# Optimization experiments

Measured on AMD Instinct MI355X. Metric: run time of the kernel, lower is better.

Reference implementation:

```python
import jax, jax.numpy as jnp
import numpy as np


def setup_inputs() -> dict:
    key = jax.random.key(0)
    ks = jax.random.split(key, 9)
    B, C, H, W = 4, 256, 64, 64
    Ci = C // 2
    s = 0.05  # keep activations numerically tame
    return {
        "x": jax.random.normal(ks[0], (B, C, H, W), jnp.float32),
        "w_g": jax.random.normal(ks[1], (Ci, C), jnp.float32) * s,
        "b_g": jax.random.normal(ks[2], (Ci,), jnp.float32) * s,
        "w_theta": jax.random.normal(ks[3], (Ci, C), jnp.float32) * s,
        "b_theta": jax.random.normal(ks[4], (Ci,), jnp.float32) * s,
        "w_phi": jax.random.normal(ks[5], (Ci, C), jnp.float32) * s,
        "b_phi": jax.random.normal(ks[6], (Ci,), jnp.float32) * s,
        "w_out": jax.random.normal(ks[7], (C, Ci), jnp.float32) * s,
        "b_out": jax.random.normal(ks[8], (C,), jnp.float32) * s,
    }


def reference(x, w_g, b_g, w_theta, b_theta, w_phi, b_phi, w_out, b_out):
    B, C, H, W = x.shape
    Ci = w_g.shape[0]
    N = H * W
    xr = x.reshape(B, C, N)  # flatten spatial dims

    def proj(w, b):  # 1x1 conv == per-pixel GEMM
        return jnp.einsum("oc,bcn->bon", w, xr) + b[None, :, None]

    g_x = proj(w_g, b_g)          # [B, Ci, N]
    theta_x = proj(w_theta, b_theta)
    phi_x = proj(w_phi, b_phi)

    scale = jnp.asarray(Ci, x.dtype) ** 0.5
    f = jnp.einsum("bci,bcj->bij", theta_x, phi_x) / scale  # [B, N, N]
    attn = jax.nn.softmax(f, axis=-1)

    # out[b,c,i] = sum_j g_x[b,c,j] * attn[b,i,j]
    out = jnp.einsum("bcj,bij->bci", g_x, attn)             # [B, Ci, N]
    y = jnp.einsum("oc,bcn->bon", w_out, out) + b_out[None, :, None]
    return y.reshape(B, C, H, W) + x
```

## Files before the change

kernel.cpp:

```cpp
#include <hip/hip_runtime.h>
#include <hip/hip_bf16.h>


typedef float f32x4 __attribute__((ext_vector_type(4)));
typedef float f32x16 __attribute__((ext_vector_type(16)));
typedef short s16x8 __attribute__((ext_vector_type(8)));
typedef short s16x4 __attribute__((ext_vector_type(4)));

#define B_  4
#define C_  256
#define CI_ 128
#define N_  4096

#define OFF_Q    (8ull  << 20)
#define OFF_K    (12ull << 20)
#define OFF_G    (16ull << 20)
#define OFF_O    (20ull << 20)
#define OFF_WQK  (24ull << 20)
#define OFF_WG   (OFF_WQK + 131072)
#define OFF_WOUT (OFF_WG  + 65536)
#define OFF_BQK  (OFF_WOUT + 65536)
#define OFF_BG   (OFF_BQK + 1024)
#define OFF_BOUT (OFF_BG  + 512)
#define OFF_END  (OFF_BOUT + 1024)

__device__ inline f32x4 mfma16(s16x8 a, s16x8 b, f32x4 c) {
    return __builtin_amdgcn_mfma_f32_16x16x32_bf16(a, b, c, 0, 0, 0);
}
__device__ inline f32x16 mfma32(s16x8 a, s16x8 b, f32x16 c) {
    return __builtin_amdgcn_mfma_f32_32x32x16_bf16(a, b, c, 0, 0, 0);
}
__device__ inline f32x16 mfma32f8(long a, long b, f32x16 c) {
    return __builtin_amdgcn_mfma_f32_32x32x16_fp8_fp8(a, b, c, 0, 0, 0);
}
__device__ inline s16x8 ld8(const __hip_bfloat16* p) { return *(const s16x8*)p; }
__device__ inline float b2f(short u) {
    return __uint_as_float(((unsigned int)(unsigned short)u) << 16);
}
__device__ inline unsigned int pk2(float a, float b) {
    __hip_bfloat162 h;
    h.x = __float2bfloat16(a); h.y = __float2bfloat16(b);
    return *(unsigned int*)&h;
}
__device__ inline unsigned char f2fp8(float v) {
    int r = __builtin_amdgcn_cvt_pk_fp8_f32(v, v, 0, false);
    return (unsigned char)(r & 0xff);
}
__device__ inline void gload_lds16(const void* g, void* l) {
    __builtin_amdgcn_global_load_lds(
        (const __attribute__((address_space(1))) unsigned int*)g,
        (__attribute__((address_space(3))) unsigned int*)l, 16, 0, 0);
}
__device__ inline float fexp2(float x) { return __builtin_amdgcn_exp2f(x); }

__global__ void prep_weights(const float* wg, const float* bg,
                             const float* wt, const float* bt,
                             const float* wp, const float* bp,
                             const float* wo, const float* bo, char* ws) {
    __hip_bfloat16* Wqk  = (__hip_bfloat16*)(ws + OFF_WQK);
    __hip_bfloat16* Wg   = (__hip_bfloat16*)(ws + OFF_WG);
    __hip_bfloat16* Wout = (__hip_bfloat16*)(ws + OFF_WOUT);
    float* Bqk  = (float*)(ws + OFF_BQK);
    float* Bg   = (float*)(ws + OFF_BG);
    float* Bout = (float*)(ws + OFF_BOUT);
    const float rs16 = 0.08838834764831845f * 1.4426950408889634f * 16.0f;
    int idx = blockIdx.x * 256 + threadIdx.x;
    if (idx < 65536) {
        int r = idx >> 8, c = idx & 255;
        float v = (r < 128) ? wt[r * 256 + c] * rs16 : wp[(r - 128) * 256 + c];
        Wqk[idx] = __float2bfloat16(v);
    }
    if (idx < 32768) {
        Wg[idx]   = __float2bfloat16(wg[idx]);
        Wout[idx] = __float2bfloat16(wo[idx]);
    }
    if (idx < 256) { Bqk[idx] = (idx < 128) ? bt[idx] * rs16 : bp[idx - 128]; Bout[idx] = bo[idx]; }
    if (idx < 128) Bg[idx] = bg[idx];
}

__global__ __launch_bounds__(256) void proj(const float* x, char* ws) {
    const __hip_bfloat16* Wqk = (const __hip_bfloat16*)(ws + OFF_WQK);
    const __hip_bfloat16* Wg  = (const __hip_bfloat16*)(ws + OFF_WG);
    const float* Bqk = (const float*)(ws + OFF_BQK);
    const float* Bg  = (const float*)(ws + OFF_BG);
    unsigned char* Qf = (unsigned char*)(ws + OFF_Q);
    unsigned char* Kt = (unsigned char*)(ws + OFF_K);
    __hip_bfloat16* G = (__hip_bfloat16*)(ws + OFF_G);

    __shared__ char at[32 * 512];

    int b = blockIdx.y, n0 = blockIdx.x * 32;
    int t = threadIdx.x;
    int w = t >> 6, l = t & 63, lr = l & 15, lg = l >> 4;

    {
        int n4 = (t & 7) * 4;
        int cp = t >> 3;
        const float* xb = x + ((size_t)b * C_) * N_ + n0 + n4;
#pragma unroll
        for (int p = 0; p < 4; p++) {
            int c0 = (p * 32 + cp) * 2;
            f32x4 vA = *(const f32x4*)(xb + (size_t)c0 * N_);
            f32x4 vB = *(const f32x4*)(xb + (size_t)(c0 + 1) * N_);
            int slot = c0 >> 3, coff = (c0 & 7) << 1;
#pragma unroll
            for (int i = 0; i < 4; i++) {
                int n = n4 + i;
                *(unsigned int*)(&at[n * 512 + ((slot ^ (n & 7)) << 4) + coff]) =
                    pk2(vA[i], vB[i]);
            }
        }
    }
    __syncthreads();

    f32x4 acc[4][2] = {};
    f32x4 accg[2][2] = {};
    int o0q = w * 64, o0g = w * 32;
#pragma unroll
    for (int kk = 0; kk < 8; kk++) {
        s16x8 a[2];
#pragma unroll
        for (int nf = 0; nf < 2; nf++) {
            int row = nf * 16 + lr;
            int s = (4 * kk + lg) ^ (row & 7);
            a[nf] = *(const s16x8*)(&at[row * 512 + s * 16]);
        }
#pragma unroll
        for (int of = 0; of < 4; of++) {
            s16x8 bb = ld8(Wqk + (size_t)(o0q + 16 * of + lr) * C_ + kk * 32 + lg * 8);
            acc[of][0] = mfma16(a[0], bb, acc[of][0]);
            acc[of][1] = mfma16(a[1], bb, acc[of][1]);
        }
#pragma unroll
        for (int og = 0; og < 2; og++) {
            s16x8 ag = ld8(Wg + (size_t)(o0g + 16 * og + lr) * C_ + kk * 32 + lg * 8);
            accg[og][0] = mfma16(ag, a[0], accg[og][0]);
            accg[og][1] = mfma16(ag, a[1], accg[og][1]);
        }
    }
#pragma unroll
    for (int of = 0; of < 4; of++) {
        int o = o0q + 16 * of + lr;
        float bias = Bqk[o];
#pragma unroll
        for (int nf = 0; nf < 2; nf++) {
#pragma unroll
            for (int i = 0; i < 4; i++) {
                int n = n0 + 16 * nf + lg * 4 + i;
                float v = acc[of][nf][i] + bias;
                unsigned char u8 = f2fp8(v);
                if (o < 128) {
                    Qf[((size_t)b * N_ + n) * 128 + o] = u8;
                } else {
                    int op = o - 128;
                    size_t a2 = (((size_t)b * (N_ / 32) + (n >> 5)) << 12) +
                                ((op >> 3) << 8) + ((n & 31) << 3) + (op & 7);
                    Kt[a2] = u8;
                }
            }
        }
    }
#pragma unroll
    for (int og = 0; og < 2; og++) {
#pragma unroll
        for (int i = 0; i < 4; i++) {
            int o = o0g + 16 * og + lg * 4 + i;
            float bias = Bg[o];
#pragma unroll
            for (int nf = 0; nf < 2; nf++) {
                int n = n0 + 16 * nf + lr;
                G[(size_t)(b * CI_ + o) * N_ + n] = __float2bfloat16(accg[og][nf][i] + bias);
            }
        }
    }
}

__global__ __launch_bounds__(256, 4) void flashf8(char* ws, int nchunk,
                                                  unsigned long long off_part,
                                                  unsigned long long off_ml) {
    const unsigned char* Qf = (const unsigned char*)(ws + OFF_Q);
    const unsigned char* Kt = (const unsigned char*)(ws + OFF_K);
    const __hip_bfloat16* G = (const __hip_bfloat16*)(ws + OFF_G);
    __hip_bfloat16* OP = (__hip_bfloat16*)(ws + off_part);
    float* ML = (float*)(ws + off_ml);

    __shared__ char kbuf[2][4096];
    __shared__ char vbuf[2][128 * 64];

    int L = blockIdx.x;
    int npairs = B_ * nchunk;
    int pair = L % npairs, qt = L / npairs;
    int b = pair / nchunk, cz = pair % nchunk;
    int per = 128 / nchunk, rem = 128 % nchunk;
    int jb_t = per * cz + (cz < rem ? cz : rem);
    int sz_t = per + (cz < rem ? 1 : 0);
    int jb = jb_t << 5, je = jb + (sz_t << 5);

    int w = threadIdx.x >> 6, l = threadIdx.x & 63;
    int cl = l & 31, hi = l >> 5;
    int q0 = qt * 128 + w * 32;
    int vkey = (l >> 1) & 3;

    auto STAGE = [&](int pb_, int j0_) {
        {
            const char* src = (const char*)Kt +
                (((size_t)b * (N_ / 32) + (j0_ >> 5)) << 12) + w * 1024 + (l << 4);
            gload_lds16(src, &kbuf[pb_][w * 1024]);
        }
#pragma unroll
        for (int i = 0; i < 2; i++) {
            int c = w * 32 + i * 16 + (l >> 2);
            int srcslot = (l & 3) ^ ((l >> 3) & 3);
            const char* src = (const char*)G + ((((size_t)b * CI_ + c) * N_ + j0_) << 1)
                              + (srcslot << 4);
            gload_lds16(src, &vbuf[pb_][(w * 32 + i * 16) * 64]);
        }
    };

    long qf[8];
    {
        const char* qrow = (const char*)Qf + ((size_t)b * N_ + q0 + cl) * 128 + hi * 8;
#pragma unroll
        for (int st = 0; st < 8; st++) qf[st] = *(const long*)(qrow + st * 16);
    }

    f32x16 oacc[4] = {};
    float m_i = 0.f, lsum = 0.f, negmc = 0.f;

    STAGE(0, jb);
    __syncthreads();
    int pb = 0;

    for (int j0 = jb; j0 < je; j0 += 32) {
        if (j0 + 32 < je) STAGE(pb ^ 1, j0 + 32);
        const char* kb = kbuf[pb];
        const char* vbb = vbuf[pb];
        f32x16 s = {};
        __builtin_amdgcn_s_setprio(1);
#pragma unroll
        for (int st = 0; st < 8; st++) {
            long kf = *(const long*)(kb + (((st << 1) + hi) << 8) + (cl << 3));
            s = mfma32f8(kf, qf[st], s);
        }
        __builtin_amdgcn_s_setprio(0);
        if (j0 == jb) {
            float t0 = fmaxf(fmaxf(s[0], s[1]), fmaxf(s[2], s[3]));
            float t1 = fmaxf(fmaxf(s[4], s[5]), fmaxf(s[6], s[7]));
            float t2 = fmaxf(fmaxf(s[8], s[9]), fmaxf(s[10], s[11]));
            float t3 = fmaxf(fmaxf(s[12], s[13]), fmaxf(s[14], s[15]));
            float tm = fmaxf(fmaxf(t0, t1), fmaxf(t2, t3));
            tm = fmaxf(tm, __shfl_xor(tm, 32));
            m_i = tm;
            negmc = -m_i * 0.0625f;
        }
#pragma unroll
        for (int r = 0; r < 16; r++) s[r] = fexp2(fmaf(s[r], 0.0625f, negmc));
        lsum += ((s[0] + s[1]) + (s[2] + s[3])) + ((s[4] + s[5]) + (s[6] + s[7]))
              + ((s[8] + s[9]) + (s[10] + s[11])) + ((s[12] + s[13]) + (s[14] + s[15]));
        union { unsigned int u[4]; s16x8 v; } pa0, pa1;
#pragma unroll
        for (int i = 0; i < 4; i++) {
            pa0.u[i] = pk2(s[2 * i], s[2 * i + 1]);
            pa1.u[i] = pk2(s[8 + 2 * i], s[9 + 2 * i]);
        }
        __builtin_amdgcn_s_setprio(1);
#pragma unroll
        for (int u = 0; u < 2; u++) {
            s16x8 pa = u ? pa1.v : pa0.v;
#pragma unroll
            for (int cb = 0; cb < 4; cb++) {
                const char* base = vbb + ((cb * 32 + cl) << 6) + hi * 8;
                union { s16x4 h[2]; s16x8 v; } vf;
                vf.h[0] = *(const s16x4*)(base + ((((u << 1))     ^ vkey) << 4));
                vf.h[1] = *(const s16x4*)(base + ((((u << 1) | 1) ^ vkey) << 4));
                oacc[cb] = mfma32(pa, vf.v, oacc[cb]);
            }
        }
        __builtin_amdgcn_s_setprio(0);
        __syncthreads();
        pb ^= 1;
    }
    lsum += __shfl_xor(lsum, 32);
#pragma unroll
    for (int cb = 0; cb < 4; cb++) {
#pragma unroll
        for (int r = 0; r < 16; r++) {
            int q = q0 + (r & 3) + 8 * (r >> 2) + 4 * hi;
            OP[((size_t)(cz * B_ + b) * N_ + q) * CI_ + cb * 32 + cl] =
                __float2bfloat16(oacc[cb][r]);
        }
    }
    if (l < 32) {
        size_t mi = ((size_t)(cz * B_ + b) * N_ + q0 + l) * 2;
        ML[mi] = m_i * 0.0625f;
        ML[mi + 1] = lsum;
    }
}

template <int NC>
__global__ __launch_bounds__(256) void combine(char* ws,
                                               unsigned long long off_part,
                                               unsigned long long off_ml) {
    const __hip_bfloat16* OP = (const __hip_bfloat16*)(ws + off_part);
    const float* ML = (const float*)(ws + off_ml);
    __hip_bfloat16* O = (__hip_bfloat16*)(ws + OFF_O);
    int idx = blockIdx.x * 256 + threadIdx.x;
    int cg = idx & 15, n = (idx >> 4) & (N_ - 1), b = idx >> 16;
    float mz[NC], lz[NC], M = -1e30f;
#pragma unroll
    for (int z = 0; z < NC; z++) {
        size_t mi = ((size_t)(z * B_ + b) * N_ + n) * 2;
        mz[z] = ML[mi]; lz[z] = ML[mi + 1];
        M = fmaxf(M, mz[z]);
    }
    float Lsum = 0.f, wz[NC];
#pragma unroll
    for (int z = 0; z < NC; z++) { wz[z] = fexp2(mz[z] - M); Lsum += lz[z] * wz[z]; }
    float inv = 1.f / Lsum;
    float o[8] = {};
#pragma unroll
    for (int z = 0; z < NC; z++) {
        s16x8 v = ld8(OP + ((size_t)(z * B_ + b) * N_ + n) * CI_ + cg * 8);
        float wv = wz[z] * inv;
#pragma unroll
        for (int i = 0; i < 8; i++) o[i] += wv * b2f(v[i]);
    }
    s16x8 r;
#pragma unroll
    for (int i = 0; i < 8; i++) {
        __hip_bfloat16 h = __float2bfloat16(o[i]);
        r[i] = *(short*)&h;
    }
    *(s16x8*)(O + ((size_t)b * N_ + n) * CI_ + cg * 8) = r;
}

__global__ __launch_bounds__(256) void gemm_out(const float* x, char* ws, float* y) {
    const __hip_bfloat16* Ob = (const __hip_bfloat16*)(ws + OFF_O);
    const __hip_bfloat16* Wo = (const __hip_bfloat16*)(ws + OFF_WOUT);
    const float* Bout = (const float*)(ws + OFF_BOUT);
    int b = blockIdx.y;
    int w = threadIdx.x >> 6, l = threadIdx.x & 63, lr = l & 15, lg = l >> 4;
    int n0 = blockIdx.x * 32;
    int o0 = w * 64;
    f32x4 acc[4][2] = {};
#pragma unroll
    for (int kk = 0; kk < 4; kk++) {
        s16x8 bb[2];
#pragma unroll
        for (int nf = 0; nf < 2; nf++)
            bb[nf] = ld8(Ob + (size_t)(b * N_ + n0 + 16 * nf + lr) * CI_ + kk * 32 + lg * 8);
#pragma unroll
        for (int of = 0; of < 4; of++) {
            s16x8 a = ld8(Wo + (size_t)(o0 + 16 * of + lr) * CI_ + kk * 32 + lg * 8);
#pragma unroll
            for (int nf = 0; nf < 2; nf++)
                acc[of][nf] = mfma16(a, bb[nf], acc[of][nf]);
        }
    }
#pragma unroll
    for (int of = 0; of < 4; of++) {
#pragma unroll
        for (int i = 0; i < 4; i++) {
            int o = o0 + 16 * of + lg * 4 + i;
            float bias = Bout[o];
#pragma unroll
            for (int nf = 0; nf < 2; nf++) {
                int n = n0 + 16 * nf + lr;
                size_t idx = (size_t)(b * C_ + o) * N_ + n;
                y[idx] = acc[of][nf][i] + bias + x[idx];
            }
        }
    }
}

extern "C" void kernel_launch(void* const* d_in, const int* in_sizes, int n_in,
                              void* d_out, int out_size, void* d_ws, size_t ws_size,
                              hipStream_t stream) {
    const float* x  = (const float*)d_in[0];
    const float* wg = (const float*)d_in[1];
    const float* bg = (const float*)d_in[2];
    const float* wt = (const float*)d_in[3];
    const float* bt = (const float*)d_in[4];
    const float* wp = (const float*)d_in[5];
    const float* bp = (const float*)d_in[6];
    const float* wo = (const float*)d_in[7];
    const float* bo = (const float*)d_in[8];
    char* ws = (char*)d_ws;
    float* y = (float*)d_out;

    unsigned long long need8 = OFF_END + (32ull << 20) + (2ull << 20);
    unsigned long long need4 = OFF_END + (16ull << 20) + (1ull << 20);
    int nchunk;
    unsigned long long off_part, off_ml;
    if (ws_size >= need8) {
        nchunk = 8; off_part = OFF_END; off_ml = OFF_END + (32ull << 20);
    } else if (ws_size >= need4) {
        nchunk = 4; off_part = OFF_END; off_ml = OFF_END + (16ull << 20);
    } else {
        nchunk = 2; off_part = 0ull; off_ml = OFF_END;
    }

    prep_weights<<<256, 256, 0, stream>>>(wg, bg, wt, bt, wp, bp, wo, bo, ws);
    proj<<<dim3(128, 4), 256, 0, stream>>>(x, ws);
    flashf8<<<dim3(32 * B_ * nchunk), 256, 0, stream>>>(ws, nchunk, off_part, off_ml);
    if (nchunk == 8)      combine<8><<<1024, 256, 0, stream>>>(ws, off_part, off_ml);
    else if (nchunk == 4) combine<4><<<1024, 256, 0, stream>>>(ws, off_part, off_ml);
    else                  combine<2><<<1024, 256, 0, stream>>>(ws, off_part, off_ml);
    gemm_out<<<dim3(128, 4), 256, 0, stream>>>(x, ws, y);
}
```

Before: 91.12 us.

## Store V as FP8 in tiled layout and use FP8 MFMA for PV

The projection kernel now writes the value tensor G as FP8 in a key-tile-blocked transposed layout instead of BF16 row-major. The attention kernel stages V with a single 16-byte async load per lane, and packs the softmax probabilities to FP8 so the PV product uses the FP8 32x32x16 MFMA instead of BF16. This halves V traffic and LDS footprint and doubles MFMA throughput for PV, at the cost of reduced precision in the probabilities and values. The old XOR-swizzle for the V buffer is dropped, so LDS bank conflicts may change.

Result: faster. 85.36 us (-6.3%).

```diff
diff --git a/kernel.cpp b/kernel.cpp
--- a/kernel.cpp
+++ b/kernel.cpp
@@ -5,7 +5,6 @@
 typedef float f32x4 __attribute__((ext_vector_type(4)));
 typedef float f32x16 __attribute__((ext_vector_type(16)));
 typedef short s16x8 __attribute__((ext_vector_type(8)));
-typedef short s16x4 __attribute__((ext_vector_type(4)));
 
 #define B_  4
 #define C_  256
@@ -26,9 +25,6 @@
 
 __device__ inline f32x4 mfma16(s16x8 a, s16x8 b, f32x4 c) {
     return __builtin_amdgcn_mfma_f32_16x16x32_bf16(a, b, c, 0, 0, 0);
-}
-__device__ inline f32x16 mfma32(s16x8 a, s16x8 b, f32x16 c) {
-    return __builtin_amdgcn_mfma_f32_32x32x16_bf16(a, b, c, 0, 0, 0);
 }
 __device__ inline f32x16 mfma32f8(long a, long b, f32x16 c) {
     return __builtin_amdgcn_mfma_f32_32x32x16_fp8_fp8(a, b, c, 0, 0, 0);
@@ -85,7 +81,7 @@
     const float* Bg  = (const float*)(ws + OFF_BG);
     unsigned char* Qf = (unsigned char*)(ws + OFF_Q);
     unsigned char* Kt = (unsigned char*)(ws + OFF_K);
-    __hip_bfloat16* G = (__hip_bfloat16*)(ws + OFF_G);
+    unsigned char* Gt = (unsigned char*)(ws + OFF_G);
 
     __shared__ char at[32 * 512];
 
@@ -169,23 +165,26 @@
 #pragma unroll
             for (int nf = 0; nf < 2; nf++) {
                 int n = n0 + 16 * nf + lr;
-                G[(size_t)(b * CI_ + o) * N_ + n] = __float2bfloat16(accg[og][nf][i] + bias);
+                float v = accg[og][nf][i] + bias;
+                size_t a3 = (((size_t)b * (N_ / 32) + (n >> 5)) << 12) +
+                            (((n & 31) >> 3) << 10) + (o << 3) + (n & 7);
+                Gt[a3] = f2fp8(v);
             }
         }
     }
 }
 
-__global__ __launch_bounds__(256, 4) void flashf8(char* ws, int nchunk,
-                                                  unsigned long long off_part,
-                                                  unsigned long long off_ml) {
+__global__ __launch_bounds__(256, 4) void flashf8b(char* ws, int nchunk,
+                                                   unsigned long long off_part,
+                                                   unsigned long long off_ml) {
     const unsigned char* Qf = (const unsigned char*)(ws + OFF_Q);
     const unsigned char* Kt = (const unsigned char*)(ws + OFF_K);
-    const __hip_bfloat16* G = (const __hip_bfloat16*)(ws + OFF_G);
+    const unsigned char* Gt = (const unsigned char*)(ws + OFF_G);
     __hip_bfloat16* OP = (__hip_bfloat16*)(ws + off_part);
     float* ML = (float*)(ws + off_ml);
 
     __shared__ char kbuf[2][4096];
-    __shared__ char vbuf[2][128 * 64];
+    __shared__ char vbuf[2][4096];
 
     int L = blockIdx.x;
     int npairs = B_ * nchunk;
@@ -199,7 +198,6 @@
     int w = threadIdx.x >> 6, l = threadIdx.x & 63;
     int cl = l & 31, hi = l >> 5;
     int q0 = qt * 128 + w * 32;
-    int vkey = (l >> 1) & 3;
 
     auto STAGE = [&](int pb_, int j0_) {
         {
@@ -207,13 +205,10 @@
                 (((size_t)b * (N_ / 32) + (j0_ >> 5)) << 12) + w * 1024 + (l << 4);
             gload_lds16(src, &kbuf[pb_][w * 1024]);
         }
-#pragma unroll
-        for (int i = 0; i < 2; i++) {
-            int c = w * 32 + i * 16 + (l >> 2);
-            int srcslot = (l & 3) ^ ((l >> 3) & 3);
-            const char* src = (const char*)G + ((((size_t)b * CI_ + c) * N_ + j0_) << 1)
-                              + (srcslot << 4);
-            gload_lds16(src, &vbuf[pb_][(w * 32 + i * 16) * 64]);
+        {
+            const char* src = (const char*)Gt +
+                (((size_t)b * (N_ / 32) + (j0_ >> 5)) << 12) + w * 1024 + (l << 4);
+            gload_lds16(src, &vbuf[pb_][w * 1024]);
         }
     };
 
@@ -257,23 +252,34 @@
         for (int r = 0; r < 16; r++) s[r] = fexp2(fmaf(s[r], 0.0625f, negmc));
         lsum += ((s[0] + s[1]) + (s[2] + s[3])) + ((s[4] + s[5]) + (s[6] + s[7]))
               + ((s[8] + s[9]) + (s[10] + s[11])) + ((s[12] + s[13]) + (s[14] + s[15]));
-        union { unsigned int u[4]; s16x8 v; } pa0, pa1;
-#pragma unroll
-        for (int i = 0; i < 4; i++) {
-            pa0.u[i] = pk2(s[2 * i], s[2 * i + 1]);
-            pa1.u[i] = pk2(s[8 + 2 * i], s[9 + 2 * i]);
+        long pa01[2];
+        {
+            int u0 = __builtin_amdgcn_cvt_pk_fp8_f32(s[0], s[1], 0, false);
+            u0     = __builtin_amdgcn_cvt_pk_fp8_f32(s[2], s[3], u0, true);
+            int u1 = __builtin_amdgcn_cvt_pk_fp8_f32(s[4], s[5], 0, false);
+            u1     = __builtin_amdgcn_cvt_pk_fp8_f32(s[6], s[7], u1, true);
+            pa01[0] = (long)(((unsigned long long)(unsigned int)u1 << 32) |
+                             (unsigned int)u0);
+            int u2 = __builtin_amdgcn_cvt_pk_fp8_f32(s[8], s[9], 0, false);
+            u2     = __builtin_amdgcn_cvt_pk_fp8_f32(s[10], s[11], u2, true);
+            int u3 = __builtin_amdgcn_cvt_pk_fp8_f32(s[12], s[13], 0, false);
+            u3     = __builtin_amdgcn_cvt_pk_fp8_f32(s[14], s[15], u3, true);
+            pa01[1] = (long)(((unsigned long long)(unsigned int)u3 << 32) |
+                             (unsigned int)u2);
         }
         __builtin_amdgcn_s_setprio(1);
 #pragma unroll
         for (int u = 0; u < 2; u++) {
-            s16x8 pa = u ? pa1.v : pa0.v;
+            long pa = pa01[u];
 #pragma unroll
             for (int cb = 0; cb < 4; cb++) {
-                const char* base = vbb + ((cb * 32 + cl) << 6) + hi * 8;
-                union { s16x4 h[2]; s16x8 v; } vf;
-                vf.h[0] = *(const s16x4*)(base + ((((u << 1))     ^ vkey) << 4));
-                vf.h[1] = *(const s16x4*)(base + ((((u << 1) | 1) ^ vkey) << 4));
-                oacc[cb] = mfma32(pa, vf.v, oacc[cb]);
+                int c = cb * 32 + cl;
+                unsigned int vlo = *(const unsigned int*)(vbb + ((u << 1) << 10) +
+                                                          (c << 3) + (hi << 2));
+                unsigned int vhi = *(const unsigned int*)(vbb + (((u << 1) | 1) << 10) +
+                                                          (c << 3) + (hi << 2));
+                long vf = (long)(((unsigned long long)vhi << 32) | vlo);
+                oacc[cb] = mfma32f8(pa, vf, oacc[cb]);
             }
         }
         __builtin_amdgcn_s_setprio(0);
@@ -402,7 +408,7 @@
 
     prep_weights<<<256, 256, 0, stream>>>(wg, bg, wt, bt, wp, bp, wo, bo, ws);
     proj<<<dim3(128, 4), 256, 0, stream>>>(x, ws);
-    flashf8<<<dim3(32 * B_ * nchunk), 256, 0, stream>>>(ws, nchunk, off_part, off_ml);
+    flashf8b<<<dim3(32 * B_ * nchunk), 256, 0, stream>>>(ws, nchunk, off_part, off_ml);
     if (nchunk == 8)      combine<8><<<1024, 256, 0, stream>>>(ws, off_part, off_ml);
     else if (nchunk == 4) combine<4><<<1024, 256, 0, stream>>>(ws, off_part, off_ml);
     else                  combine<2><<<1024, 256, 0, stream>>>(ws, off_part, off_ml);
```
